# Optimization experiments

Hardware: AMD Instinct MI355X
Metric: run time of the kernel (lower is better)

The kernel has to match this reference:

```python
import jax, jax.numpy as jnp
import numpy as np

B = 16384
IN = 512
H = 512

def setup_inputs() -> dict:
    key = jax.random.key(0)
    ks = jax.random.split(key, 8)
    inp = {
        "x_t": jax.random.normal(ks[0], (B, IN), dtype=jnp.float32),
        "h_t": jax.random.normal(ks[1], (B, H), dtype=jnp.float32),
        "W_ir": jax.random.normal(ks[2], (IN, H), dtype=jnp.float32),
        "W_hr": jax.random.normal(ks[3], (H, H), dtype=jnp.float32),
        "b_r": jnp.zeros((H,), dtype=jnp.float32),
        "W_iz": jax.random.normal(ks[4], (IN, H), dtype=jnp.float32),
        "W_hz": jax.random.normal(ks[5], (H, H), dtype=jnp.float32),
        "b_z": jnp.zeros((H,), dtype=jnp.float32),
        "W_in": jax.random.normal(ks[6], (IN, H), dtype=jnp.float32),
        "W_hn": jax.random.normal(ks[7], (H, H), dtype=jnp.float32),
        "b_n": jnp.zeros((H,), dtype=jnp.float32),
    }
    return inp

def reference(x_t, h_t, W_ir, W_hr, b_r, W_iz, W_hz, b_z, W_in, W_hn, b_n):
    # Fuse the three input-side and three hidden-side GEMMs by concatenating weights.
    Wi = jnp.concatenate([W_ir, W_iz, W_in], axis=1)   # [IN, 3H]
    Wh = jnp.concatenate([W_hr, W_hz, W_hn], axis=1)   # [H, 3H]
    gi = x_t @ Wi                                      # [B, 3H]
    gh = h_t @ Wh                                      # [B, 3H]
    h = b_r.shape[0]
    r_t = jax.nn.sigmoid(gi[:, :h] + gh[:, :h] + b_r)
    z_t = jax.nn.sigmoid(gi[:, h:2*h] + gh[:, h:2*h] + b_z)
    n_t = jnp.tanh(gi[:, 2*h:] + r_t * gh[:, 2*h:] + b_n)
    return (1.0 - z_t) * n_t + z_t * h_t
```

## Files before the change

kernel.cpp:

```cpp
#include <hip/hip_runtime.h>
#include <hip/hip_fp16.h>

typedef _Float16 half8 __attribute__((ext_vector_type(8)));
typedef float floatx4 __attribute__((ext_vector_type(4)));

#define WLO_OFF (6 * 512 * 512)
#define WMAT_STRIDE ((size_t)(8 * 16 * 2048))

__global__ __launch_bounds__(256) void permute_w(
    const float* __restrict__ Wir, const float* __restrict__ Whr,
    const float* __restrict__ Wiz, const float* __restrict__ Whz,
    const float* __restrict__ Win, const float* __restrict__ Whn,
    _Float16* __restrict__ wperm) {
  __shared__ __align__(16) float tile[32 * 68];
  const int b = blockIdx.x;
  const int w = b >> 7;
  const int rem = b & 127;
  const int ki = rem >> 3;
  const int nt = rem & 7;
  const float* W = (w == 0) ? Wir : (w == 1) ? Whr : (w == 2) ? Wiz
                 : (w == 3) ? Whz : (w == 4) ? Win : Whn;
  const int k0 = ki * 32, n0 = nt * 64;
  const int t = threadIdx.x;

  const int kk = t >> 3;
  const int nn = (t & 7) * 8;
  const float* src = W + (k0 + kk) * 512 + n0 + nn;
  float4 f0 = *(const float4*)(src);
  float4 f1 = *(const float4*)(src + 4);
  float* drow = tile + kk * 68 + nn;
  *(float4*)(drow) = f0;
  *(float4*)(drow + 4) = f1;
  __syncthreads();

  const int u = t >> 6, l = t & 63;
  const int nloc = 16 * u + (l & 15);
  const int kbase = 8 * (l >> 4);
  half8 vh, vl;
#pragma unroll
  for (int j = 0; j < 8; ++j) {
    float f = tile[(kbase + j) * 68 + nloc];
    _Float16 hi = (_Float16)f;
    _Float16 lo = (_Float16)(f - (float)hi);
    vh[j] = hi;
    vl[j] = lo;
  }
  const size_t off = ((size_t)((w * 8 + nt) * 16 + ki)) * 2048 + t * 8;
  *(half8*)(wperm + off) = vh;
  *(half8*)(wperm + WLO_OFF + off) = vl;
}

__global__ __launch_bounds__(256, 2) void gru_fused(
    const float* __restrict__ x, const float* __restrict__ h,
    const _Float16* __restrict__ wperm,
    const float* __restrict__ br, const float* __restrict__ bz,
    const float* __restrict__ bn, float* __restrict__ out) {
  __shared__ __align__(16) _Float16 ldsA[2 * 4 * 4096];

  const int t = threadIdx.x;
  const int lane = t & 63;
  const int wn = t >> 6;
  const int bid = blockIdx.x;
  const int nt = bid & 7;
  const int mt = bid >> 3;
  const int m0 = mt * 128;
  const int n0 = nt * 64;
  const _Float16* wlo = wperm + WLO_OFF;

  floatx4 acc_r[8] = {};
  floatx4 acc_z[8] = {};
  floatx4 acc_in[8] = {};
  floatx4 acc_hn[8] = {};

  const int mA = 16 * (t >> 6) + (t & 15);
  const int kA = 8 * ((t >> 4) & 3);
  const float* px0 = x + (m0 + mA) * 512 + kA;
  const float* ph0 = h + (m0 + mA) * 512 + kA;
  const float* px1 = px0 + 64 * 512;
  const float* ph1 = ph0 + 64 * 512;
  const int c0 = t, c1 = t + 256;

  {
    float v[4][8];
    *(float4*)&v[0][0] = *(const float4*)(px0);
    *(float4*)&v[0][4] = *(const float4*)(px0 + 4);
    *(float4*)&v[1][0] = *(const float4*)(px1);
    *(float4*)&v[1][4] = *(const float4*)(px1 + 4);
    *(float4*)&v[2][0] = *(const float4*)(ph0);
    *(float4*)&v[2][4] = *(const float4*)(ph0 + 4);
    *(float4*)&v[3][0] = *(const float4*)(ph1);
    *(float4*)&v[3][4] = *(const float4*)(ph1 + 4);
#pragma unroll
    for (int g = 0; g < 4; ++g) {
      half8 hi, lo;
#pragma unroll
      for (int j = 0; j < 8; ++j) {
        _Float16 a = (_Float16)v[g][j];
        hi[j] = a;
        lo[j] = (_Float16)(v[g][j] - (float)a);
      }
      const int c = (g & 1) ? c1 : c0;
      const int part = (g >> 1) * 2;
      *(half8*)(ldsA + (part + 0) * 4096 + c * 8) = hi;
      *(half8*)(ldsA + (part + 1) * 4096 + c * 8) = lo;
    }
  }
  __syncthreads();

  for (int kt = 0; kt < 16; ++kt) {
    const _Float16* A = ldsA + (kt & 1) * 16384;

    const size_t tb = ((size_t)(nt * 16 + kt)) * 2048 + wn * 512 + lane * 8;
    half8 bh_ir = *(const half8*)(wperm + tb + 0 * WMAT_STRIDE);
    half8 bh_hr = *(const half8*)(wperm + tb + 1 * WMAT_STRIDE);
    half8 bh_iz = *(const half8*)(wperm + tb + 2 * WMAT_STRIDE);
    half8 bh_hz = *(const half8*)(wperm + tb + 3 * WMAT_STRIDE);
    half8 bh_in = *(const half8*)(wperm + tb + 4 * WMAT_STRIDE);
    half8 bh_hn = *(const half8*)(wperm + tb + 5 * WMAT_STRIDE);
    half8 bl_ir = *(const half8*)(wlo + tb + 0 * WMAT_STRIDE);
    half8 bl_hr = *(const half8*)(wlo + tb + 1 * WMAT_STRIDE);
    half8 bl_iz = *(const half8*)(wlo + tb + 2 * WMAT_STRIDE);
    half8 bl_hz = *(const half8*)(wlo + tb + 3 * WMAT_STRIDE);
    half8 bl_in = *(const half8*)(wlo + tb + 4 * WMAT_STRIDE);
    half8 bl_hn = *(const half8*)(wlo + tb + 5 * WMAT_STRIDE);
    __builtin_amdgcn_sched_barrier(0);

    float v[4][8];
    if (kt < 15) {
      const int k0 = (kt + 1) * 32;
      *(float4*)&v[0][0] = *(const float4*)(px0 + k0);
      *(float4*)&v[0][4] = *(const float4*)(px0 + k0 + 4);
      *(float4*)&v[1][0] = *(const float4*)(px1 + k0);
      *(float4*)&v[1][4] = *(const float4*)(px1 + k0 + 4);
      *(float4*)&v[2][0] = *(const float4*)(ph0 + k0);
      *(float4*)&v[2][4] = *(const float4*)(ph0 + k0 + 4);
      *(float4*)&v[3][0] = *(const float4*)(ph1 + k0);
      *(float4*)&v[3][4] = *(const float4*)(ph1 + k0 + 4);
    }
    __builtin_amdgcn_sched_barrier(0);

    __builtin_amdgcn_s_setprio(1);
#pragma unroll
    for (int i = 0; i < 8; ++i) {
      const int ao = (i * 64 + lane) * 8;
      half8 axh = *(const half8*)(A + 0 * 4096 + ao);
      half8 axl = *(const half8*)(A + 1 * 4096 + ao);
      half8 ahh = *(const half8*)(A + 2 * 4096 + ao);
      half8 ahl = *(const half8*)(A + 3 * 4096 + ao);
      acc_r[i]  = __builtin_amdgcn_mfma_f32_16x16x32_f16(axh, bh_ir, acc_r[i], 0, 0, 0);
      acc_r[i]  = __builtin_amdgcn_mfma_f32_16x16x32_f16(ahh, bh_hr, acc_r[i], 0, 0, 0);
      acc_z[i]  = __builtin_amdgcn_mfma_f32_16x16x32_f16(axh, bh_iz, acc_z[i], 0, 0, 0);
      acc_z[i]  = __builtin_amdgcn_mfma_f32_16x16x32_f16(ahh, bh_hz, acc_z[i], 0, 0, 0);
      acc_in[i] = __builtin_amdgcn_mfma_f32_16x16x32_f16(axh, bh_in, acc_in[i], 0, 0, 0);
      acc_hn[i] = __builtin_amdgcn_mfma_f32_16x16x32_f16(ahh, bh_hn, acc_hn[i], 0, 0, 0);
      acc_r[i]  = __builtin_amdgcn_mfma_f32_16x16x32_f16(axl, bh_ir, acc_r[i], 0, 0, 0);
      acc_r[i]  = __builtin_amdgcn_mfma_f32_16x16x32_f16(ahl, bh_hr, acc_r[i], 0, 0, 0);
      acc_z[i]  = __builtin_amdgcn_mfma_f32_16x16x32_f16(axl, bh_iz, acc_z[i], 0, 0, 0);
      acc_z[i]  = __builtin_amdgcn_mfma_f32_16x16x32_f16(ahl, bh_hz, acc_z[i], 0, 0, 0);
      acc_in[i] = __builtin_amdgcn_mfma_f32_16x16x32_f16(axl, bh_in, acc_in[i], 0, 0, 0);
      acc_hn[i] = __builtin_amdgcn_mfma_f32_16x16x32_f16(ahl, bh_hn, acc_hn[i], 0, 0, 0);
      acc_r[i]  = __builtin_amdgcn_mfma_f32_16x16x32_f16(axh, bl_ir, acc_r[i], 0, 0, 0);
      acc_r[i]  = __builtin_amdgcn_mfma_f32_16x16x32_f16(ahh, bl_hr, acc_r[i], 0, 0, 0);
      acc_z[i]  = __builtin_amdgcn_mfma_f32_16x16x32_f16(axh, bl_iz, acc_z[i], 0, 0, 0);
      acc_z[i]  = __builtin_amdgcn_mfma_f32_16x16x32_f16(ahh, bl_hz, acc_z[i], 0, 0, 0);
      acc_in[i] = __builtin_amdgcn_mfma_f32_16x16x32_f16(axh, bl_in, acc_in[i], 0, 0, 0);
      acc_hn[i] = __builtin_amdgcn_mfma_f32_16x16x32_f16(ahh, bl_hn, acc_hn[i], 0, 0, 0);
    }
    __builtin_amdgcn_s_setprio(0);

    if (kt < 15) {
      _Float16* base = ldsA + ((kt & 1) ^ 1) * 16384;
#pragma unroll
      for (int g = 0; g < 4; ++g) {
        half8 hi, lo;
#pragma unroll
        for (int j = 0; j < 8; ++j) {
          _Float16 a = (_Float16)v[g][j];
          hi[j] = a;
          lo[j] = (_Float16)(v[g][j] - (float)a);
        }
        const int c = (g & 1) ? c1 : c0;
        const int part = (g >> 1) * 2;
        *(half8*)(base + (part + 0) * 4096 + c * 8) = hi;
        *(half8*)(base + (part + 1) * 4096 + c * 8) = lo;
      }
    }
    __syncthreads();
  }

  const int quad = lane >> 4;
  const int col = lane & 15;
  const int n = n0 + wn * 16 + col;
  const float vbr = br[n], vbz = bz[n], vbn = bn[n];
#pragma unroll
  for (int i = 0; i < 8; ++i) {
    const int mbase = m0 + i * 16 + quad * 4;
#pragma unroll
    for (int r = 0; r < 4; ++r) {
      const int m = mbase + r;
      const float gr = acc_r[i][r] + vbr;
      const float gz = acc_z[i][r] + vbz;
      const float rg = 1.0f / (1.0f + __expf(-gr));
      const float zg = 1.0f / (1.0f + __expf(-gz));
      const float gn = acc_in[i][r] + rg * acc_hn[i][r] + vbn;
      const float e2 = __expf(2.0f * gn);
      const float ntv = 1.0f - 2.0f / (e2 + 1.0f);
      const float hp = h[m * 512 + n];
      out[m * 512 + n] = (1.0f - zg) * ntv + zg * hp;
    }
  }
}

extern "C" void kernel_launch(void* const* d_in, const int* in_sizes, int n_in,
                              void* d_out, int out_size, void* d_ws, size_t ws_size,
                              hipStream_t stream) {
  const float* x   = (const float*)d_in[0];
  const float* h   = (const float*)d_in[1];
  const float* Wir = (const float*)d_in[2];
  const float* Whr = (const float*)d_in[3];
  const float* br  = (const float*)d_in[4];
  const float* Wiz = (const float*)d_in[5];
  const float* Whz = (const float*)d_in[6];
  const float* bz  = (const float*)d_in[7];
  const float* Win = (const float*)d_in[8];
  const float* Whn = (const float*)d_in[9];
  const float* bn  = (const float*)d_in[10];
  float* out = (float*)d_out;
  _Float16* wperm = (_Float16*)d_ws;

  permute_w<<<768, 256, 0, stream>>>(Wir, Whr, Wiz, Whz, Win, Whn, wperm);
  gru_fused<<<1024, 256, 0, stream>>>(x, h, wperm, br, bz, bn, out);
}
```

Measured before the change: 251.8 us.

## Pre-split activations into fp16 hi/lo tiles and stream them via async LDS loads

Adds a prep kernel that converts x and h once into a pre-permuted fp16 hi/lo tile layout in workspace, merged with the weight permutation. The GEMM kernel then fills LDS with direct global-to-LDS async loads instead of loading fp32, converting and storing in every block. This removes the conversion that was repeated by each of the 8 column blocks. It also remaps block IDs so blocks sharing an M tile land on the same XCD, and unrolls the k loop by 2. The cost is an extra round trip of about 64MB through memory and a dependence on workspace size, with the old path kept as a fallback.

```diff
diff --git a/kernel.cpp b/kernel.cpp
--- a/kernel.cpp
+++ b/kernel.cpp
@@ -4,25 +4,31 @@
 typedef _Float16 half8 __attribute__((ext_vector_type(8)));
 typedef float floatx4 __attribute__((ext_vector_type(4)));
 
+#define AS1 __attribute__((address_space(1)))
+#define AS3 __attribute__((address_space(3)))
+
 #define WLO_OFF (6 * 512 * 512)
 #define WMAT_STRIDE ((size_t)(8 * 16 * 2048))
-
-__global__ __launch_bounds__(256) void permute_w(
+#define APERM_OFF ((size_t)(2 * WLO_OFF))
+#define APERM_HALFS ((size_t)128 * 16 * 4 * 4096)
+
+__device__ __forceinline__ void async_lds16(const void* g, void* l) {
+  __builtin_amdgcn_global_load_lds((const AS1 void*)g, (AS3 void*)l, 16, 0, 0);
+}
+
+__device__ __forceinline__ void permute_w_body(
+    int b2, int t,
     const float* __restrict__ Wir, const float* __restrict__ Whr,
     const float* __restrict__ Wiz, const float* __restrict__ Whz,
     const float* __restrict__ Win, const float* __restrict__ Whn,
-    _Float16* __restrict__ wperm) {
-  __shared__ __align__(16) float tile[32 * 68];
-  const int b = blockIdx.x;
-  const int w = b >> 7;
-  const int rem = b & 127;
+    _Float16* __restrict__ wperm, float* tile) {
+  const int w = b2 >> 7;
+  const int rem = b2 & 127;
   const int ki = rem >> 3;
   const int nt = rem & 7;
   const float* W = (w == 0) ? Wir : (w == 1) ? Whr : (w == 2) ? Wiz
                  : (w == 3) ? Whz : (w == 4) ? Win : Whn;
   const int k0 = ki * 32, n0 = nt * 64;
-  const int t = threadIdx.x;
-
   const int kk = t >> 3;
   const int nn = (t & 7) * 8;
   const float* src = W + (k0 + kk) * 512 + n0 + nn;
@@ -32,85 +38,112 @@
   *(float4*)(drow) = f0;
   *(float4*)(drow + 4) = f1;
   __syncthreads();
-
   const int u = t >> 6, l = t & 63;
   const int nloc = 16 * u + (l & 15);
   const int kbase = 8 * (l >> 4);
-  half8 vh, vl;
+  half8 vh2, vl2;
 #pragma unroll
   for (int j = 0; j < 8; ++j) {
     float f = tile[(kbase + j) * 68 + nloc];
     _Float16 hi = (_Float16)f;
     _Float16 lo = (_Float16)(f - (float)hi);
-    vh[j] = hi;
-    vl[j] = lo;
+    vh2[j] = hi;
+    vl2[j] = lo;
   }
   const size_t off = ((size_t)((w * 8 + nt) * 16 + ki)) * 2048 + t * 8;
-  *(half8*)(wperm + off) = vh;
-  *(half8*)(wperm + WLO_OFF + off) = vl;
-}
-
-__global__ __launch_bounds__(256, 2) void gru_fused(
+  *(half8*)(wperm + off) = vh2;
+  *(half8*)(wperm + WLO_OFF + off) = vl2;
+}
+
+__global__ __launch_bounds__(256) void prep(
     const float* __restrict__ x, const float* __restrict__ h,
-    const _Float16* __restrict__ wperm,
+    const float* __restrict__ Wir, const float* __restrict__ Whr,
+    const float* __restrict__ Wiz, const float* __restrict__ Whz,
+    const float* __restrict__ Win, const float* __restrict__ Whn,
+    _Float16* __restrict__ wperm) {
+  __shared__ __align__(16) float tile[32 * 68];
+  const int b = blockIdx.x;
+  const int t = threadIdx.x;
+
+  if (b >= 2048) {
+    permute_w_body(b - 2048, t, Wir, Whr, Wiz, Whz, Win, Whn, wperm, tile);
+    return;
+  }
+
+  const int mt = b >> 4, kt = b & 15;
+  _Float16* dst = wperm + APERM_OFF + ((size_t)(mt * 16 + kt)) * 16384;
+  const int k0 = kt * 32;
+#pragma unroll
+  for (int hc = 0; hc < 2; ++hc) {
+    const int c = t + hc * 256;
+    const int m = 16 * (c >> 6) + (c & 15);
+    const int kA = 8 * ((c >> 4) & 3);
+    const float* px = x + ((size_t)(mt * 128 + m)) * 512 + k0 + kA;
+    const float* ph = h + ((size_t)(mt * 128 + m)) * 512 + k0 + kA;
+    float vx[8], vh[8];
+    *(float4*)&vx[0] = *(const float4*)px;  *(float4*)&vx[4] = *(const float4*)(px + 4);
+    *(float4*)&vh[0] = *(const float4*)ph;  *(float4*)&vh[4] = *(const float4*)(ph + 4);
+    half8 xh, xl, hh, hl;
+#pragma unroll
+    for (int j = 0; j < 8; ++j) {
+      _Float16 a = (_Float16)vx[j];
+      xh[j] = a; xl[j] = (_Float16)(vx[j] - (float)a);
+      _Float16 bb = (_Float16)vh[j];
+      hh[j] = bb; hl[j] = (_Float16)(vh[j] - (float)bb);
+    }
+    *(half8*)(dst + 0 * 4096 + c * 8) = xh;
+    *(half8*)(dst + 1 * 4096 + c * 8) = xl;
+    *(half8*)(dst + 2 * 4096 + c * 8) = hh;
+    *(half8*)(dst + 3 * 4096 + c * 8) = hl;
+  }
+}
+
+__global__ __launch_bounds__(256) void permute_w(
+    const float* __restrict__ Wir, const float* __restrict__ Whr,
+    const float* __restrict__ Wiz, const float* __restrict__ Whz,
+    const float* __restrict__ Win, const float* __restrict__ Whn,
+    _Float16* __restrict__ wperm) {
+  __shared__ __align__(16) float tile[32 * 68];
+  permute_w_body(blockIdx.x, threadIdx.x, Wir, Whr, Wiz, Whz, Win, Whn, wperm, tile);
+}
+
+__global__ __launch_bounds__(256, 2) void gru_fused2(
+    const float* __restrict__ h, const _Float16* __restrict__ wperm,
     const float* __restrict__ br, const float* __restrict__ bz,
     const float* __restrict__ bn, float* __restrict__ out) {
   __shared__ __align__(16) _Float16 ldsA[2 * 4 * 4096];
 
   const int t = threadIdx.x;
   const int lane = t & 63;
-  const int wn = t >> 6;
+  const int wv = t >> 6;
   const int bid = blockIdx.x;
-  const int nt = bid & 7;
-  const int mt = bid >> 3;
+  const int xcd = bid & 7;
+  const int g = bid >> 3;
+  const int nt = g & 7;
+  const int mt = (g >> 3) * 8 + xcd;
   const int m0 = mt * 128;
   const int n0 = nt * 64;
   const _Float16* wlo = wperm + WLO_OFF;
+  const _Float16* aperm = wperm + APERM_OFF + (size_t)mt * 16 * 16384;
 
   floatx4 acc_r[8] = {};
   floatx4 acc_z[8] = {};
   floatx4 acc_in[8] = {};
   floatx4 acc_hn[8] = {};
 
-  const int mA = 16 * (t >> 6) + (t & 15);
-  const int kA = 8 * ((t >> 4) & 3);
-  const float* px0 = x + (m0 + mA) * 512 + kA;
-  const float* ph0 = h + (m0 + mA) * 512 + kA;
-  const float* px1 = px0 + 64 * 512;
-  const float* ph1 = ph0 + 64 * 512;
-  const int c0 = t, c1 = t + 256;
-
   {
-    float v[4][8];
-    *(float4*)&v[0][0] = *(const float4*)(px0);
-    *(float4*)&v[0][4] = *(const float4*)(px0 + 4);
-    *(float4*)&v[1][0] = *(const float4*)(px1);
-    *(float4*)&v[1][4] = *(const float4*)(px1 + 4);
-    *(float4*)&v[2][0] = *(const float4*)(ph0);
-    *(float4*)&v[2][4] = *(const float4*)(ph0 + 4);
-    *(float4*)&v[3][0] = *(const float4*)(ph1);
-    *(float4*)&v[3][4] = *(const float4*)(ph1 + 4);
-#pragma unroll
-    for (int g = 0; g < 4; ++g) {
-      half8 hi, lo;
-#pragma unroll
-      for (int j = 0; j < 8; ++j) {
-        _Float16 a = (_Float16)v[g][j];
-        hi[j] = a;
-        lo[j] = (_Float16)(v[g][j] - (float)a);
-      }
-      const int c = (g & 1) ? c1 : c0;
-      const int part = (g >> 1) * 2;
-      *(half8*)(ldsA + (part + 0) * 4096 + c * 8) = hi;
-      *(half8*)(ldsA + (part + 1) * 4096 + c * 8) = lo;
-    }
+    const _Float16* asrc = aperm + wv * 4096 + lane * 8;
+    _Float16* adst = ldsA + wv * 4096;
+#pragma unroll
+    for (int q = 0; q < 8; ++q) async_lds16(asrc + q * 512, adst + q * 512);
   }
   __syncthreads();
 
+#pragma unroll 2
   for (int kt = 0; kt < 16; ++kt) {
     const _Float16* A = ldsA + (kt & 1) * 16384;
 
-    const size_t tb = ((size_t)(nt * 16 + kt)) * 2048 + wn * 512 + lane * 8;
+    const size_t tb = ((size_t)(nt * 16 + kt)) * 2048 + wv * 512 + lane * 8;
     half8 bh_ir = *(const half8*)(wperm + tb + 0 * WMAT_STRIDE);
     half8 bh_hr = *(const half8*)(wperm + tb + 1 * WMAT_STRIDE);
     half8 bh_iz = *(const half8*)(wperm + tb + 2 * WMAT_STRIDE);
@@ -125,17 +158,12 @@
     half8 bl_hn = *(const half8*)(wlo + tb + 5 * WMAT_STRIDE);
     __builtin_amdgcn_sched_barrier(0);
 
-    float v[4][8];
     if (kt < 15) {
-      const int k0 = (kt + 1) * 32;
-      *(float4*)&v[0][0] = *(const float4*)(px0 + k0);
-      *(float4*)&v[0][4] = *(const float4*)(px0 + k0 + 4);
-      *(float4*)&v[1][0] = *(const float4*)(px1 + k0);
-      *(float4*)&v[1][4] = *(const float4*)(px1 + k0 + 4);
-      *(float4*)&v[2][0] = *(const float4*)(ph0 + k0);
-      *(float4*)&v[2][4] = *(const float4*)(ph0 + k0 + 4);
-      *(float4*)&v[3][0] = *(const float4*)(ph1 + k0);
-      *(float4*)&v[3][4] = *(const float4*)(ph1 + k0 + 4);
+      const _Float16* asrc =
+          aperm + (size_t)(kt + 1) * 16384 + wv * 4096 + lane * 8;
+      _Float16* adst = ldsA + ((kt & 1) ^ 1) * 16384 + wv * 4096;
+#pragma unroll
+      for (int q = 0; q < 8; ++q) async_lds16(asrc + q * 512, adst + q * 512);
     }
     __builtin_amdgcn_sched_barrier(0);
 
@@ -168,6 +196,141 @@
     }
     __builtin_amdgcn_s_setprio(0);
 
+    __syncthreads();
+  }
+
+  const int quad = lane >> 4;
+  const int col = lane & 15;
+  const int n = n0 + wv * 16 + col;
+  const float vbr = br[n], vbz = bz[n], vbn = bn[n];
+#pragma unroll
+  for (int i = 0; i < 8; ++i) {
+    const int mbase = m0 + i * 16 + quad * 4;
+#pragma unroll
+    for (int r = 0; r < 4; ++r) {
+      const int m = mbase + r;
+      const float gr = acc_r[i][r] + vbr;
+      const float gz = acc_z[i][r] + vbz;
+      const float rg = 1.0f / (1.0f + __expf(-gr));
+      const float zg = 1.0f / (1.0f + __expf(-gz));
+      const float gn = acc_in[i][r] + rg * acc_hn[i][r] + vbn;
+      const float e2 = __expf(2.0f * gn);
+      const float ntv = 1.0f - 2.0f / (e2 + 1.0f);
+      const float hp = h[m * 512 + n];
+      out[m * 512 + n] = (1.0f - zg) * ntv + zg * hp;
+    }
+  }
+}
+
+__global__ __launch_bounds__(256, 2) void gru_fused_fb(
+    const float* __restrict__ x, const float* __restrict__ h,
+    const _Float16* __restrict__ wperm,
+    const float* __restrict__ br, const float* __restrict__ bz,
+    const float* __restrict__ bn, float* __restrict__ out) {
+  __shared__ __align__(16) _Float16 ldsA[2 * 4 * 4096];
+  const int t = threadIdx.x;
+  const int lane = t & 63;
+  const int wn = t >> 6;
+  const int bid = blockIdx.x;
+  const int nt = bid & 7;
+  const int mt = bid >> 3;
+  const int m0 = mt * 128;
+  const int n0 = nt * 64;
+  const _Float16* wlo = wperm + WLO_OFF;
+
+  floatx4 acc_r[8] = {};
+  floatx4 acc_z[8] = {};
+  floatx4 acc_in[8] = {};
+  floatx4 acc_hn[8] = {};
+
+  const int mA = 16 * (t >> 6) + (t & 15);
+  const int kA = 8 * ((t >> 4) & 3);
+  const float* px0 = x + (m0 + mA) * 512 + kA;
+  const float* ph0 = h + (m0 + mA) * 512 + kA;
+  const float* px1 = px0 + 64 * 512;
+  const float* ph1 = ph0 + 64 * 512;
+  const int c0 = t, c1 = t + 256;
+
+  {
+    float v[4][8];
+    *(float4*)&v[0][0] = *(const float4*)(px0); *(float4*)&v[0][4] = *(const float4*)(px0 + 4);
+    *(float4*)&v[1][0] = *(const float4*)(px1); *(float4*)&v[1][4] = *(const float4*)(px1 + 4);
+    *(float4*)&v[2][0] = *(const float4*)(ph0); *(float4*)&v[2][4] = *(const float4*)(ph0 + 4);
+    *(float4*)&v[3][0] = *(const float4*)(ph1); *(float4*)&v[3][4] = *(const float4*)(ph1 + 4);
+#pragma unroll
+    for (int g = 0; g < 4; ++g) {
+      half8 hi, lo;
+#pragma unroll
+      for (int j = 0; j < 8; ++j) {
+        _Float16 a = (_Float16)v[g][j];
+        hi[j] = a;
+        lo[j] = (_Float16)(v[g][j] - (float)a);
+      }
+      const int c = (g & 1) ? c1 : c0;
+      const int part = (g >> 1) * 2;
+      *(half8*)(ldsA + (part + 0) * 4096 + c * 8) = hi;
+      *(half8*)(ldsA + (part + 1) * 4096 + c * 8) = lo;
+    }
+  }
+  __syncthreads();
+
+#pragma unroll 2
+  for (int kt = 0; kt < 16; ++kt) {
+    const _Float16* A = ldsA + (kt & 1) * 16384;
+    const size_t tb = ((size_t)(nt * 16 + kt)) * 2048 + wn * 512 + lane * 8;
+    half8 bh_ir = *(const half8*)(wperm + tb + 0 * WMAT_STRIDE);
+    half8 bh_hr = *(const half8*)(wperm + tb + 1 * WMAT_STRIDE);
+    half8 bh_iz = *(const half8*)(wperm + tb + 2 * WMAT_STRIDE);
+    half8 bh_hz = *(const half8*)(wperm + tb + 3 * WMAT_STRIDE);
+    half8 bh_in = *(const half8*)(wperm + tb + 4 * WMAT_STRIDE);
+    half8 bh_hn = *(const half8*)(wperm + tb + 5 * WMAT_STRIDE);
+    half8 bl_ir = *(const half8*)(wlo + tb + 0 * WMAT_STRIDE);
+    half8 bl_hr = *(const half8*)(wlo + tb + 1 * WMAT_STRIDE);
+    half8 bl_iz = *(const half8*)(wlo + tb + 2 * WMAT_STRIDE);
+    half8 bl_hz = *(const half8*)(wlo + tb + 3 * WMAT_STRIDE);
+    half8 bl_in = *(const half8*)(wlo + tb + 4 * WMAT_STRIDE);
+    half8 bl_hn = *(const half8*)(wlo + tb + 5 * WMAT_STRIDE);
+    __builtin_amdgcn_sched_barrier(0);
+
+    float v[4][8];
+    if (kt < 15) {
+      const int k0 = (kt + 1) * 32;
+      *(float4*)&v[0][0] = *(const float4*)(px0 + k0); *(float4*)&v[0][4] = *(const float4*)(px0 + k0 + 4);
+      *(float4*)&v[1][0] = *(const float4*)(px1 + k0); *(float4*)&v[1][4] = *(const float4*)(px1 + k0 + 4);
+      *(float4*)&v[2][0] = *(const float4*)(ph0 + k0); *(float4*)&v[2][4] = *(const float4*)(ph0 + k0 + 4);
+      *(float4*)&v[3][0] = *(const float4*)(ph1 + k0); *(float4*)&v[3][4] = *(const float4*)(ph1 + k0 + 4);
+    }
+    __builtin_amdgcn_sched_barrier(0);
+
+    __builtin_amdgcn_s_setprio(1);
+#pragma unroll
+    for (int i = 0; i < 8; ++i) {
+      const int ao = (i * 64 + lane) * 8;
+      half8 axh = *(const half8*)(A + 0 * 4096 + ao);
+      half8 axl = *(const half8*)(A + 1 * 4096 + ao);
+      half8 ahh = *(const half8*)(A + 2 * 4096 + ao);
+      half8 ahl = *(const half8*)(A + 3 * 4096 + ao);
+      acc_r[i]  = __builtin_amdgcn_mfma_f32_16x16x32_f16(axh, bh_ir, acc_r[i], 0, 0, 0);
+      acc_r[i]  = __builtin_amdgcn_mfma_f32_16x16x32_f16(ahh, bh_hr, acc_r[i], 0, 0, 0);
+      acc_z[i]  = __builtin_amdgcn_mfma_f32_16x16x32_f16(axh, bh_iz, acc_z[i], 0, 0, 0);
+      acc_z[i]  = __builtin_amdgcn_mfma_f32_16x16x32_f16(ahh, bh_hz, acc_z[i], 0, 0, 0);
+      acc_in[i] = __builtin_amdgcn_mfma_f32_16x16x32_f16(axh, bh_in, acc_in[i], 0, 0, 0);
+      acc_hn[i] = __builtin_amdgcn_mfma_f32_16x16x32_f16(ahh, bh_hn, acc_hn[i], 0, 0, 0);
+      acc_r[i]  = __builtin_amdgcn_mfma_f32_16x16x32_f16(axl, bh_ir, acc_r[i], 0, 0, 0);
+      acc_r[i]  = __builtin_amdgcn_mfma_f32_16x16x32_f16(ahl, bh_hr, acc_r[i], 0, 0, 0);
+      acc_z[i]  = __builtin_amdgcn_mfma_f32_16x16x32_f16(axl, bh_iz, acc_z[i], 0, 0, 0);
+      acc_z[i]  = __builtin_amdgcn_mfma_f32_16x16x32_f16(ahl, bh_hz, acc_z[i], 0, 0, 0);
+      acc_in[i] = __builtin_amdgcn_mfma_f32_16x16x32_f16(axl, bh_in, acc_in[i], 0, 0, 0);
+      acc_hn[i] = __builtin_amdgcn_mfma_f32_16x16x32_f16(ahl, bh_hn, acc_hn[i], 0, 0, 0);
+      acc_r[i]  = __builtin_amdgcn_mfma_f32_16x16x32_f16(axh, bl_ir, acc_r[i], 0, 0, 0);
+      acc_r[i]  = __builtin_amdgcn_mfma_f32_16x16x32_f16(ahh, bl_hr, acc_r[i], 0, 0, 0);
+      acc_z[i]  = __builtin_amdgcn_mfma_f32_16x16x32_f16(axh, bl_iz, acc_z[i], 0, 0, 0);
+      acc_z[i]  = __builtin_amdgcn_mfma_f32_16x16x32_f16(ahh, bl_hz, acc_z[i], 0, 0, 0);
+      acc_in[i] = __builtin_amdgcn_mfma_f32_16x16x32_f16(axh, bl_in, acc_in[i], 0, 0, 0);
+      acc_hn[i] = __builtin_amdgcn_mfma_f32_16x16x32_f16(ahh, bl_hn, acc_hn[i], 0, 0, 0);
+    }
+    __builtin_amdgcn_s_setprio(0);
+
     if (kt < 15) {
       _Float16* base = ldsA + ((kt & 1) ^ 1) * 16384;
 #pragma unroll
@@ -228,6 +391,12 @@
   float* out = (float*)d_out;
   _Float16* wperm = (_Float16*)d_ws;
 
-  permute_w<<<768, 256, 0, stream>>>(Wir, Whr, Wiz, Whz, Win, Whn, wperm);
-  gru_fused<<<1024, 256, 0, stream>>>(x, h, wperm, br, bz, bn, out);
-}
+  const size_t need_bytes = (APERM_OFF + APERM_HALFS) * 2;
+  if (ws_size >= need_bytes) {
+    prep<<<2816, 256, 0, stream>>>(x, h, Wir, Whr, Wiz, Whz, Win, Whn, wperm);
+    gru_fused2<<<1024, 256, 0, stream>>>(h, wperm, br, bz, bn, out);
+  } else {
+    permute_w<<<768, 256, 0, stream>>>(Wir, Whr, Wiz, Whz, Win, Whn, wperm);
+    gru_fused_fb<<<1024, 256, 0, stream>>>(x, h, wperm, br, bz, bn, out);
+  }
+}
```

Measured after the change: 263.2 us. +4.5%, slower.
